# Optimization experiments

Measured on AMD Instinct MI355X. Metric: run time of the kernel, lower is better.

Reference implementation:

```python
import jax, jax.numpy as jnp
import numpy as np

B, T, S, H = 32, 1, 4096, 1024

def setup_inputs() -> dict:
    key = jax.random.key(0)
    ks = jax.random.split(key, 8)
    query = jax.random.normal(ks[0], (B, T, H), dtype=jnp.float32)
    encoder_outputs = jax.random.normal(ks[1], (B, S, H), dtype=jnp.float32)
    src_lengths = jax.random.randint(ks[2], (B,), 1, S + 1, dtype=jnp.int64)
    sc = 1.0 / np.sqrt(H)
    Ws_w = jax.random.normal(ks[3], (H, H), dtype=jnp.float32) * sc   # torch Linear weight (out,in)
    Wh_w = jax.random.normal(ks[4], (H, H), dtype=jnp.float32) * sc
    v_w = jax.random.normal(ks[5], (1, H), dtype=jnp.float32) * sc
    Wout_w = jax.random.normal(ks[6], (H, 2 * H), dtype=jnp.float32) * sc
    return {"query": query, "encoder_outputs": encoder_outputs, "src_lengths": src_lengths,
            "Ws_w": Ws_w, "Wh_w": Wh_w, "v_w": v_w, "Wout_w": Wout_w}

def reference(query, encoder_outputs, src_lengths, Ws_w, Wh_w, v_w, Wout_w):
    # score(h, s) = v^T tanh(Ws q + Wh h); query is a single decoder step (T=1)
    q_proj = jnp.einsum('bth,oh->bto', query, Ws_w)            # (B,1,H)
    h_proj = jnp.einsum('bsh,oh->bso', encoder_outputs, Wh_w)  # (B,S,H)
    scores = jnp.einsum('bsh,h->bs', jnp.tanh(q_proj + h_proj), v_w[0])  # (B,S)
    # NOTE: original calls non-in-place masked_fill and discards the result,
    # so src_lengths has no effect on the output (replicated faithfully).
    attn = jax.nn.softmax(scores, axis=-1)                     # (B,S)
    ctx = jnp.einsum('bs,bsh->bh', attn, encoder_outputs)[:, None, :]  # (B,1,H)
    cat = jnp.concatenate([ctx, query], axis=-1)               # (B,1,2H)
    return jnp.tanh(jnp.einsum('btk,ok->bto', cat, Wout_w))    # (B,1,H)
```

## Files before the change

kernel.cpp:

```cpp
#include <hip/hip_runtime.h>
#include <hip/hip_bf16.h>

#define B_  32
#define S_  4096
#define H_  1024
#define M_  (B_*S_)

typedef __attribute__((ext_vector_type(8))) short bf16x8;
typedef __attribute__((ext_vector_type(4))) float f32x4;

typedef void __attribute__((address_space(3)))* lds_ptr_t;
typedef void __attribute__((address_space(1)))* gbl_ptr_t;

__device__ __forceinline__ unsigned short f2bf(float x) {
    return __builtin_bit_cast(unsigned short, __float2bfloat16(x));
}

__device__ __forceinline__ float tanh_fast(float x) {
    float e = __expf(2.0f * x);
    return 1.0f - 2.0f / (e + 1.0f);
}

__global__ __launch_bounds__(256) void k_cvt_bf16(const float* __restrict__ in,
                                                  unsigned short* __restrict__ out, int n4) {
    int i = blockIdx.x * 256 + threadIdx.x;
    if (i < n4) {
        float4 f = reinterpret_cast<const float4*>(in)[i];
        ushort4 u;
        u.x = f2bf(f.x); u.y = f2bf(f.y); u.z = f2bf(f.z); u.w = f2bf(f.w);
        reinterpret_cast<ushort4*>(out)[i] = u;
    }
}

__global__ __launch_bounds__(256) void k_qproj(const float* __restrict__ q,
                                               const float* __restrict__ Ws,
                                               float* __restrict__ qp) {
    const int b = blockIdx.y, oc = blockIdx.x, tid = threadIdx.x;
    __shared__ float ql[H_];
    for (int i = tid; i < H_; i += 256) ql[i] = q[b*H_ + i];
    __syncthreads();
    const int o = oc*256 + tid;
    const float4* w = reinterpret_cast<const float4*>(&Ws[(size_t)o * H_]);
    float acc = 0.f;
    #pragma unroll 4
    for (int k4 = 0; k4 < H_/4; ++k4) {
        float4 ww = w[k4];
        acc += ql[k4*4+0]*ww.x + ql[k4*4+1]*ww.y + ql[k4*4+2]*ww.z + ql[k4*4+3]*ww.w;
    }
    qp[b*H_ + o] = acc;
}

__global__ __launch_bounds__(256) void k_scores(const float* __restrict__ enc,
                                                const unsigned short* __restrict__ whb,
                                                const float* __restrict__ qp,
                                                const float* __restrict__ vw,
                                                float* __restrict__ sp) {
    __shared__ __align__(16) unsigned short As[2][128][32];
    __shared__ __align__(16) unsigned short Bs[2][128][32];
    __shared__ float sred[2][128];

    const int tid  = threadIdx.x;
    const int lane = tid & 63;
    const int wid  = tid >> 6;
    const int wr = wid >> 1, wc = wid & 1;
    const int fr = lane & 15;
    const int fk = (lane >> 4) * 8;

    const int bn = blockIdx.x;
    const int bm = blockIdx.y;
    const int row0 = bm * 128;
    const int col0 = bn * 128;
    const int b = row0 >> 12;

    const int ar = tid >> 3;
    const int ak = (tid & 7) * 4;
    const int bnr = tid >> 2;
    const int bkk = (tid & 3) * 8;

    float4 areg[4];

    auto loadA = [&](int kt) {
        #pragma unroll
        for (int p = 0; p < 4; ++p)
            areg[p] = *reinterpret_cast<const float4*>(
                &enc[(size_t)(row0 + p*32 + ar) * H_ + kt*32 + ak]);
    };
    auto writeA = [&](int buf) {
        #pragma unroll
        for (int p = 0; p < 4; ++p) {
            ushort4 u;
            u.x = f2bf(areg[p].x); u.y = f2bf(areg[p].y);
            u.z = f2bf(areg[p].z); u.w = f2bf(areg[p].w);
            *reinterpret_cast<ushort4*>(&As[buf][p*32 + ar][ak]) = u;
        }
    };
    auto stageB = [&](int buf, int kt) {
        const unsigned short* g0 = whb + (size_t)(col0 + bnr) * H_ + kt*32 + bkk;
        const unsigned short* g1 = g0 + (size_t)64 * H_;
        char* l0 = (char*)(&Bs[buf][0][0]) + tid*16;
        __builtin_amdgcn_global_load_lds((gbl_ptr_t)g0, (lds_ptr_t)l0,        16, 0, 0);
        __builtin_amdgcn_global_load_lds((gbl_ptr_t)g1, (lds_ptr_t)(l0+4096), 16, 0, 0);
    };

    f32x4 acc[4][4] = {};

    loadA(0);
    stageB(0, 0);
    writeA(0);
    __syncthreads();

    for (int kt = 0; kt < 32; ++kt) {
        const int cur = kt & 1, nxt = cur ^ 1;
        if (kt < 31) { stageB(nxt, kt + 1); loadA(kt + 1); }

        bf16x8 af[4], bfr[4];
        #pragma unroll
        for (int i = 0; i < 4; ++i) {
            af[i]  = *reinterpret_cast<const bf16x8*>(&As[cur][wr*64 + i*16 + fr][fk]);
            bfr[i] = *reinterpret_cast<const bf16x8*>(&Bs[cur][wc*64 + i*16 + fr][fk]);
        }
        #pragma unroll
        for (int i = 0; i < 4; ++i)
            #pragma unroll
            for (int j = 0; j < 4; ++j)
                acc[i][j] = __builtin_amdgcn_mfma_f32_16x16x32_bf16(af[i], bfr[j], acc[i][j], 0, 0, 0);

        if (kt < 31) writeA(nxt);
        __syncthreads();
    }

    float vv[4], qq[4];
    #pragma unroll
    for (int j = 0; j < 4; ++j) {
        int c = col0 + wc*64 + j*16 + fr;
        vv[j] = vw[c];
        qq[j] = qp[b*H_ + c];
    }
    #pragma unroll
    for (int i = 0; i < 4; ++i) {
        #pragma unroll
        for (int r = 0; r < 4; ++r) {
            float s = 0.f;
            #pragma unroll
            for (int j = 0; j < 4; ++j)
                s += vv[j] * tanh_fast(qq[j] + acc[i][j][r]);
            #pragma unroll
            for (int m = 1; m < 16; m <<= 1)
                s += __shfl_xor(s, m, 64);
            if (fr == 0)
                sred[wc][wr*64 + i*16 + (lane >> 4)*4 + r] = s;
        }
    }
    __syncthreads();
    if (tid < 128)
        sp[(size_t)bn * M_ + row0 + tid] = sred[0][tid] + sred[1][tid];
}

__global__ __launch_bounds__(256) void k_softmax(const float* __restrict__ sp,
                                                 float* __restrict__ attn) {
    const int b = blockIdx.x, tid = threadIdx.x;
    __shared__ float red[4];
    float vals[16];
    float mx = -1e30f;
    #pragma unroll
    for (int i = 0; i < 16; ++i) {
        int s = i*256 + tid;
        float x = 0.f;
        #pragma unroll
        for (int p = 0; p < 8; ++p) x += sp[(size_t)p*M_ + b*S_ + s];
        vals[i] = x;
        mx = fmaxf(mx, x);
    }
    #pragma unroll
    for (int m = 1; m < 64; m <<= 1) mx = fmaxf(mx, __shfl_xor(mx, m, 64));
    if ((tid & 63) == 0) red[tid >> 6] = mx;
    __syncthreads();
    mx = fmaxf(fmaxf(red[0], red[1]), fmaxf(red[2], red[3]));
    float sum = 0.f;
    #pragma unroll
    for (int i = 0; i < 16; ++i) { vals[i] = __expf(vals[i] - mx); sum += vals[i]; }
    #pragma unroll
    for (int m = 1; m < 64; m <<= 1) sum += __shfl_xor(sum, m, 64);
    __syncthreads();
    if ((tid & 63) == 0) red[tid >> 6] = sum;
    __syncthreads();
    sum = red[0] + red[1] + red[2] + red[3];
    float inv = 1.f / sum;
    #pragma unroll
    for (int i = 0; i < 16; ++i) attn[b*S_ + i*256 + tid] = vals[i] * inv;
}

__global__ __launch_bounds__(256) void k_ctx(const float* __restrict__ attn,
                                             const float* __restrict__ enc,
                                             float* __restrict__ ctxp) {
    const int sc = blockIdx.x;
    const int b  = blockIdx.y;
    const int h  = threadIdx.x * 4;
    float ax = 0.f, ay = 0.f, az = 0.f, aw = 0.f;
    const int s0 = sc * 256;
    #pragma unroll 4
    for (int s = s0; s < s0 + 256; ++s) {
        float a = attn[b*S_ + s];
        float4 e = *reinterpret_cast<const float4*>(&enc[((size_t)b*S_ + s) * H_ + h]);
        ax += a*e.x; ay += a*e.y; az += a*e.z; aw += a*e.w;
    }
    float4 o; o.x = ax; o.y = ay; o.z = az; o.w = aw;
    *reinterpret_cast<float4*>(&ctxp[((size_t)sc*B_ + b) * H_ + h]) = o;
}

__global__ __launch_bounds__(256) void k_out(const float* __restrict__ ctxp,
                                             const float* __restrict__ q,
                                             const float* __restrict__ Wout,
                                             float* __restrict__ out) {
    const int oc = blockIdx.x, b = blockIdx.y, tid = threadIdx.x;
    __shared__ float cat[2*H_];
    for (int k = tid; k < H_; k += 256) {
        float s = 0.f;
        #pragma unroll
        for (int p = 0; p < 16; ++p) s += ctxp[((size_t)p*B_ + b) * H_ + k];
        cat[k] = s;
        cat[H_ + k] = q[b*H_ + k];
    }
    __syncthreads();
    const int o = oc*256 + tid;
    const float4* w = reinterpret_cast<const float4*>(&Wout[(size_t)o * 2*H_]);
    float acc = 0.f;
    #pragma unroll 4
    for (int k4 = 0; k4 < 2*H_/4; ++k4) {
        float4 ww = w[k4];
        acc += cat[k4*4+0]*ww.x + cat[k4*4+1]*ww.y + cat[k4*4+2]*ww.z + cat[k4*4+3]*ww.w;
    }
    out[b*H_ + o] = tanh_fast(acc);
}

extern "C" void kernel_launch(void* const* d_in, const int* in_sizes, int n_in,
                              void* d_out, int out_size, void* d_ws, size_t ws_size,
                              hipStream_t stream) {
    const float* query = (const float*)d_in[0];
    const float* enc   = (const float*)d_in[1];
    const float* Ws    = (const float*)d_in[3];
    const float* Wh    = (const float*)d_in[4];
    const float* vw    = (const float*)d_in[5];
    const float* Wout  = (const float*)d_in[6];
    float* out = (float*)d_out;

    char* ws = (char*)d_ws;
    unsigned short* whb = (unsigned short*)ws;
    float* sp   = (float*)(ws + (2u  << 20));
    float* attn = (float*)(ws + (6u  << 20));
    float* qp   = (float*)(ws + (6u  << 20) + (512u << 10));
    float* ctxp = (float*)(ws + (7u  << 20));

    k_cvt_bf16<<<dim3(1024),   dim3(256), 0, stream>>>(Wh, whb, H_*H_/4);
    k_qproj   <<<dim3(4, 32),  dim3(256), 0, stream>>>(query, Ws, qp);
    k_scores  <<<dim3(8, 1024),dim3(256), 0, stream>>>(enc, whb, qp, vw, sp);
    k_softmax <<<dim3(32),     dim3(256), 0, stream>>>(sp, attn);
    k_ctx     <<<dim3(16, 32), dim3(256), 0, stream>>>(attn, enc, ctxp);
    k_out     <<<dim3(4, 32),  dim3(256), 0, stream>>>(ctxp, query, Wout, out);
}
```

Baseline: 782.9 us.

## Pre-convert encoder outputs to bf16 and stage GEMM tiles via direct global-to-LDS loads

Adds a pass that converts the whole fp32 encoder tensor to bf16 in workspace. The scores GEMM then streams bf16 A tiles with global_load_lds, and the context reduction reads bf16 instead of fp32. This removes the per-tile fp32-to-bf16 conversion and eight-fold re-reads of fp32 data across the column blocks. It also remaps the 1D grid so blocks sharing rows run together for L2 reuse. The cost is an extra 512MB read plus 256MB write for conversion, a workspace requirement of about 266MB, and bf16 rounding in the context sum.

```diff
diff --git a/kernel.cpp b/kernel.cpp
--- a/kernel.cpp
+++ b/kernel.cpp
@@ -8,6 +8,7 @@
 
 typedef __attribute__((ext_vector_type(8))) short bf16x8;
 typedef __attribute__((ext_vector_type(4))) float f32x4;
+typedef __attribute__((ext_vector_type(8))) unsigned short ushort8;
 
 typedef void __attribute__((address_space(3)))* lds_ptr_t;
 typedef void __attribute__((address_space(1)))* gbl_ptr_t;
@@ -15,7 +16,9 @@
 __device__ __forceinline__ unsigned short f2bf(float x) {
     return __builtin_bit_cast(unsigned short, __float2bfloat16(x));
 }
-
+__device__ __forceinline__ float bf2f(unsigned short u) {
+    return __builtin_bit_cast(float, (unsigned)u << 16);
+}
 __device__ __forceinline__ float tanh_fast(float x) {
     float e = __expf(2.0f * x);
     return 1.0f - 2.0f / (e + 1.0f);
@@ -32,6 +35,19 @@
     }
 }
 
+__global__ __launch_bounds__(256) void k_cvt_enc(const float* __restrict__ in,
+                                                 unsigned short* __restrict__ out, int n8) {
+    const int stride = gridDim.x * 256;
+    for (int i = blockIdx.x * 256 + threadIdx.x; i < n8; i += stride) {
+        float4 a = reinterpret_cast<const float4*>(in)[(size_t)i * 2];
+        float4 b = reinterpret_cast<const float4*>(in)[(size_t)i * 2 + 1];
+        ushort8 u;
+        u[0] = f2bf(a.x); u[1] = f2bf(a.y); u[2] = f2bf(a.z); u[3] = f2bf(a.w);
+        u[4] = f2bf(b.x); u[5] = f2bf(b.y); u[6] = f2bf(b.z); u[7] = f2bf(b.w);
+        reinterpret_cast<ushort8*>(out)[i] = u;
+    }
+}
+
 __global__ __launch_bounds__(256) void k_qproj(const float* __restrict__ q,
                                                const float* __restrict__ Ws,
                                                float* __restrict__ qp) {
@@ -50,11 +66,11 @@
     qp[b*H_ + o] = acc;
 }
 
-__global__ __launch_bounds__(256) void k_scores(const float* __restrict__ enc,
-                                                const unsigned short* __restrict__ whb,
-                                                const float* __restrict__ qp,
-                                                const float* __restrict__ vw,
-                                                float* __restrict__ sp) {
+__global__ __launch_bounds__(256) void k_scores_b(const unsigned short* __restrict__ encb,
+                                                  const unsigned short* __restrict__ whb,
+                                                  const float* __restrict__ qp,
+                                                  const float* __restrict__ vw,
+                                                  float* __restrict__ sp) {
     __shared__ __align__(16) unsigned short As[2][128][32];
     __shared__ __align__(16) unsigned short Bs[2][128][32];
     __shared__ float sred[2][128];
@@ -66,8 +82,99 @@
     const int fr = lane & 15;
     const int fk = (lane >> 4) * 8;
 
-    const int bn = blockIdx.x;
-    const int bm = blockIdx.y;
+    const int h  = blockIdx.x;
+    const int L  = (h & 7) * 1024 + (h >> 3);
+    const int bm = L >> 3;
+    const int bn = L & 7;
+    const int row0 = bm * 128;
+    const int col0 = bn * 128;
+    const int b = row0 >> 12;
+
+    const int sr = tid >> 2;
+    const int sk = (tid & 3) * 8;
+
+    auto stage = [&](int buf, int kt) {
+        const unsigned short* ga0 = encb + (size_t)(row0 + sr) * H_ + kt*32 + sk;
+        const unsigned short* gb0 = whb  + (size_t)(col0 + sr) * H_ + kt*32 + sk;
+        char* la = (char*)(&As[buf][0][0]) + tid*16;
+        char* lb = (char*)(&Bs[buf][0][0]) + tid*16;
+        __builtin_amdgcn_global_load_lds((gbl_ptr_t)ga0,                 (lds_ptr_t)la,        16, 0, 0);
+        __builtin_amdgcn_global_load_lds((gbl_ptr_t)(ga0 + (size_t)64*H_),(lds_ptr_t)(la+4096), 16, 0, 0);
+        __builtin_amdgcn_global_load_lds((gbl_ptr_t)gb0,                 (lds_ptr_t)lb,        16, 0, 0);
+        __builtin_amdgcn_global_load_lds((gbl_ptr_t)(gb0 + (size_t)64*H_),(lds_ptr_t)(lb+4096), 16, 0, 0);
+    };
+
+    f32x4 acc[4][4] = {};
+
+    stage(0, 0);
+    __syncthreads();
+
+    for (int kt = 0; kt < 32; ++kt) {
+        const int cur = kt & 1, nxt = cur ^ 1;
+        if (kt < 31) stage(nxt, kt + 1);
+
+        bf16x8 af[4], bfr[4];
+        #pragma unroll
+        for (int i = 0; i < 4; ++i) {
+            af[i]  = *reinterpret_cast<const bf16x8*>(&As[cur][wr*64 + i*16 + fr][fk]);
+            bfr[i] = *reinterpret_cast<const bf16x8*>(&Bs[cur][wc*64 + i*16 + fr][fk]);
+        }
+        #pragma unroll
+        for (int i = 0; i < 4; ++i)
+            #pragma unroll
+            for (int j = 0; j < 4; ++j)
+                acc[i][j] = __builtin_amdgcn_mfma_f32_16x16x32_bf16(af[i], bfr[j], acc[i][j], 0, 0, 0);
+
+        __syncthreads();
+    }
+
+    float vv[4], qq[4];
+    #pragma unroll
+    for (int j = 0; j < 4; ++j) {
+        int c = col0 + wc*64 + j*16 + fr;
+        vv[j] = vw[c];
+        qq[j] = qp[b*H_ + c];
+    }
+    #pragma unroll
+    for (int i = 0; i < 4; ++i) {
+        #pragma unroll
+        for (int r = 0; r < 4; ++r) {
+            float s = 0.f;
+            #pragma unroll
+            for (int j = 0; j < 4; ++j)
+                s += vv[j] * tanh_fast(qq[j] + acc[i][j][r]);
+            #pragma unroll
+            for (int m = 1; m < 16; m <<= 1)
+                s += __shfl_xor(s, m, 64);
+            if (fr == 0)
+                sred[wc][wr*64 + i*16 + (lane >> 4)*4 + r] = s;
+        }
+    }
+    __syncthreads();
+    if (tid < 128)
+        sp[(size_t)bn * M_ + row0 + tid] = sred[0][tid] + sred[1][tid];
+}
+
+__global__ __launch_bounds__(256) void k_scores_f(const float* __restrict__ enc,
+                                                  const unsigned short* __restrict__ whb,
+                                                  const float* __restrict__ qp,
+                                                  const float* __restrict__ vw,
+                                                  float* __restrict__ sp) {
+    __shared__ __align__(16) unsigned short As[2][128][32];
+    __shared__ __align__(16) unsigned short Bs[2][128][32];
+    __shared__ float sred[2][128];
+
+    const int tid  = threadIdx.x;
+    const int lane = tid & 63;
+    const int wid  = tid >> 6;
+    const int wr = wid >> 1, wc = wid & 1;
+    const int fr = lane & 15;
+    const int fk = (lane >> 4) * 8;
+
+    const int h  = blockIdx.x;
+    const int L  = (h & 7) * 1024 + (h >> 3);
+    const int bm = L >> 3;
+    const int bn = L & 7;
     const int row0 = bm * 128;
     const int col0 = bn * 128;
     const int b = row0 >> 12;
@@ -78,7 +185,6 @@
     const int bkk = (tid & 3) * 8;
 
     float4 areg[4];
-
     auto loadA = [&](int kt) {
         #pragma unroll
         for (int p = 0; p < 4; ++p)
@@ -190,22 +296,40 @@
     for (int i = 0; i < 16; ++i) attn[b*S_ + i*256 + tid] = vals[i] * inv;
 }
 
-__global__ __launch_bounds__(256) void k_ctx(const float* __restrict__ attn,
-                                             const float* __restrict__ enc,
-                                             float* __restrict__ ctxp) {
+__global__ __launch_bounds__(256) void k_ctx_b(const float* __restrict__ attn,
+                                               const unsigned short* __restrict__ encb,
+                                               float* __restrict__ ctxp) {
     const int sc = blockIdx.x;
     const int b  = blockIdx.y;
-    const int h  = threadIdx.x * 4;
+    const int hh = threadIdx.x * 4;
     float ax = 0.f, ay = 0.f, az = 0.f, aw = 0.f;
     const int s0 = sc * 256;
     #pragma unroll 4
     for (int s = s0; s < s0 + 256; ++s) {
         float a = attn[b*S_ + s];
-        float4 e = *reinterpret_cast<const float4*>(&enc[((size_t)b*S_ + s) * H_ + h]);
+        ushort4 e = *reinterpret_cast<const ushort4*>(&encb[((size_t)b*S_ + s) * H_ + hh]);
+        ax += a*bf2f(e.x); ay += a*bf2f(e.y); az += a*bf2f(e.z); aw += a*bf2f(e.w);
+    }
+    float4 o; o.x = ax; o.y = ay; o.z = az; o.w = aw;
+    *reinterpret_cast<float4*>(&ctxp[((size_t)sc*B_ + b) * H_ + hh]) = o;
+}
+
+__global__ __launch_bounds__(256) void k_ctx_f(const float* __restrict__ attn,
+                                               const float* __restrict__ enc,
+                                               float* __restrict__ ctxp) {
+    const int sc = blockIdx.x;
+    const int b  = blockIdx.y;
+    const int hh = threadIdx.x * 4;
+    float ax = 0.f, ay = 0.f, az = 0.f, aw = 0.f;
+    const int s0 = sc * 256;
+    #pragma unroll 4
+    for (int s = s0; s < s0 + 256; ++s) {
+        float a = attn[b*S_ + s];
+        float4 e = *reinterpret_cast<const float4*>(&enc[((size_t)b*S_ + s) * H_ + hh]);
         ax += a*e.x; ay += a*e.y; az += a*e.z; aw += a*e.w;
     }
     float4 o; o.x = ax; o.y = ay; o.z = az; o.w = aw;
-    *reinterpret_cast<float4*>(&ctxp[((size_t)sc*B_ + b) * H_ + h]) = o;
+    *reinterpret_cast<float4*>(&ctxp[((size_t)sc*B_ + b) * H_ + hh]) = o;
 }
 
 __global__ __launch_bounds__(256) void k_out(const float* __restrict__ ctxp,
@@ -245,16 +369,34 @@
     float* out = (float*)d_out;
 
     char* ws = (char*)d_ws;
-    unsigned short* whb = (unsigned short*)ws;
-    float* sp   = (float*)(ws + (2u  << 20));
-    float* attn = (float*)(ws + (6u  << 20));
-    float* qp   = (float*)(ws + (6u  << 20) + (512u << 10));
-    float* ctxp = (float*)(ws + (7u  << 20));
-
-    k_cvt_bf16<<<dim3(1024),   dim3(256), 0, stream>>>(Wh, whb, H_*H_/4);
-    k_qproj   <<<dim3(4, 32),  dim3(256), 0, stream>>>(query, Ws, qp);
-    k_scores  <<<dim3(8, 1024),dim3(256), 0, stream>>>(enc, whb, qp, vw, sp);
-    k_softmax <<<dim3(32),     dim3(256), 0, stream>>>(sp, attn);
-    k_ctx     <<<dim3(16, 32), dim3(256), 0, stream>>>(attn, enc, ctxp);
-    k_out     <<<dim3(4, 32),  dim3(256), 0, stream>>>(ctxp, query, Wout, out);
-}
+
+    if (ws_size >= (266ull << 20)) {
+        unsigned short* encb = (unsigned short*)ws;
+        unsigned short* whb  = (unsigned short*)(ws + (256ull << 20));
+        float* sp   = (float*)(ws + (258ull << 20));
+        float* attn = (float*)(ws + (262ull << 20));
+        float* qp   = (float*)(ws + (262ull << 20) + (512u << 10));
+        float* ctxp = (float*)(ws + (263ull << 20));
+
+        k_cvt_enc <<<dim3(2048),    dim3(256), 0, stream>>>(enc, encb, M_*H_/8);
+        k_cvt_bf16<<<dim3(1024),    dim3(256), 0, stream>>>(Wh, whb, H_*H_/4);
+        k_qproj   <<<dim3(4, 32),   dim3(256), 0, stream>>>(query, Ws, qp);
+        k_scores_b<<<dim3(8192),    dim3(256), 0, stream>>>(encb, whb, qp, vw, sp);
+        k_softmax <<<dim3(32),      dim3(256), 0, stream>>>(sp, attn);
+        k_ctx_b   <<<dim3(16, 32),  dim3(256), 0, stream>>>(attn, encb, ctxp);
+        k_out     <<<dim3(4, 32),   dim3(256), 0, stream>>>(ctxp, query, Wout, out);
+    } else {
+        unsigned short* whb = (unsigned short*)ws;
+        float* sp   = (float*)(ws + (2u  << 20));
+        float* attn = (float*)(ws + (6u  << 20));
+        float* qp   = (float*)(ws + (6u  << 20) + (512u << 10));
+        float* ctxp = (float*)(ws + (7u  << 20));
+
+        k_cvt_bf16<<<dim3(1024),    dim3(256), 0, stream>>>(Wh, whb, H_*H_/4);
+        k_qproj   <<<dim3(4, 32),   dim3(256), 0, stream>>>(query, Ws, qp);
+        k_scores_f<<<dim3(8192),    dim3(256), 0, stream>>>(enc, whb, qp, vw, sp);
+        k_softmax <<<dim3(32),      dim3(256), 0, stream>>>(sp, attn);
+        k_ctx_f   <<<dim3(16, 32),  dim3(256), 0, stream>>>(attn, enc, ctxp);
+        k_out     <<<dim3(4, 32),   dim3(256), 0, stream>>>(ctxp, query, Wout, out);
+    }
+}
```

Measured after the change: 672.0 us. 14.2% less time.

## Rewrite scores GEMM with fragment-native LDS layout and deeper prefetch pipeline

Applied to the files above, without the earlier changes.

Rewrites the scores GEMM kernel. LDS tiles are now laid out in MFMA fragment order, A is prefetched two stages ahead in registers, and B uses a triple-buffered global_load_lds ring. Syncs are manual waitcnt plus s_barrier, MFMA blocks are wrapped in s_setprio, and the 1-D grid is remapped so blocks sharing the same column tile of Wh are spread across the launch order. The aim is to hide global-load latency, avoid LDS bank conflicts, and raise occupancy via launch bounds (256,3), at the cost of more registers and fragile hand-tuned wait counts.

```diff
diff --git a/kernel.cpp b/kernel.cpp
--- a/kernel.cpp
+++ b/kernel.cpp
@@ -8,6 +8,7 @@
 
 typedef __attribute__((ext_vector_type(8))) short bf16x8;
 typedef __attribute__((ext_vector_type(4))) float f32x4;
+typedef __attribute__((ext_vector_type(8))) unsigned short ushort8;
 
 typedef void __attribute__((address_space(3)))* lds_ptr_t;
 typedef void __attribute__((address_space(1)))* gbl_ptr_t;
@@ -15,7 +16,6 @@
 __device__ __forceinline__ unsigned short f2bf(float x) {
     return __builtin_bit_cast(unsigned short, __float2bfloat16(x));
 }
-
 __device__ __forceinline__ float tanh_fast(float x) {
     float e = __expf(2.0f * x);
     return 1.0f - 2.0f / (e + 1.0f);
@@ -50,114 +50,144 @@
     qp[b*H_ + o] = acc;
 }
 
-__global__ __launch_bounds__(256) void k_scores(const float* __restrict__ enc,
-                                                const unsigned short* __restrict__ whb,
-                                                const float* __restrict__ qp,
-                                                const float* __restrict__ vw,
-                                                float* __restrict__ sp) {
-    __shared__ __align__(16) unsigned short As[2][128][32];
-    __shared__ __align__(16) unsigned short Bs[2][128][32];
-    __shared__ float sred[2][128];
-
-    const int tid  = threadIdx.x;
-    const int lane = tid & 63;
-    const int wid  = tid >> 6;
-    const int wr = wid >> 1, wc = wid & 1;
-    const int fr = lane & 15;
-    const int fk = (lane >> 4) * 8;
-
-    const int bn = blockIdx.x;
-    const int bm = blockIdx.y;
+__global__ __launch_bounds__(256, 3) void k_scores_r(const float* __restrict__ enc,
+                                                     const unsigned short* __restrict__ whb,
+                                                     const float* __restrict__ qp,
+                                                     const float* __restrict__ vw,
+                                                     float* __restrict__ sp) {
+    __shared__ __align__(1024) char smem[40960];
+
+    const int tid = threadIdx.x;
+    const int l   = tid & 63;
+    const int w   = tid >> 6;
+    const int wr  = w >> 1;
+    const int wc  = w & 1;
+    const int fr  = l & 15;
+    const int fh  = l >> 4;
+
+    const int hb = blockIdx.x;
+    const int L  = (hb & 7) * 1024 + (hb >> 3);
+    const int bm = L >> 3;
+    const int bn = L & 7;
     const int row0 = bm * 128;
     const int col0 = bn * 128;
     const int b = row0 >> 12;
 
-    const int ar = tid >> 3;
-    const int ak = (tid & 7) * 4;
-    const int bnr = tid >> 2;
-    const int bkk = (tid & 3) * 8;
-
-    float4 areg[4];
-
-    auto loadA = [&](int kt) {
-        #pragma unroll
-        for (int p = 0; p < 4; ++p)
-            areg[p] = *reinterpret_cast<const float4*>(
-                &enc[(size_t)(row0 + p*32 + ar) * H_ + kt*32 + ak]);
-    };
-    auto writeA = [&](int buf) {
-        #pragma unroll
-        for (int p = 0; p < 4; ++p) {
-            ushort4 u;
-            u.x = f2bf(areg[p].x); u.y = f2bf(areg[p].y);
-            u.z = f2bf(areg[p].z); u.w = f2bf(areg[p].w);
-            *reinterpret_cast<ushort4*>(&As[buf][p*32 + ar][ak]) = u;
-        }
-    };
-    auto stageB = [&](int buf, int kt) {
-        const unsigned short* g0 = whb + (size_t)(col0 + bnr) * H_ + kt*32 + bkk;
-        const unsigned short* g1 = g0 + (size_t)64 * H_;
-        char* l0 = (char*)(&Bs[buf][0][0]) + tid*16;
-        __builtin_amdgcn_global_load_lds((gbl_ptr_t)g0, (lds_ptr_t)l0,        16, 0, 0);
-        __builtin_amdgcn_global_load_lds((gbl_ptr_t)g1, (lds_ptr_t)(l0+4096), 16, 0, 0);
-    };
-
-    f32x4 acc[4][4] = {};
-
-    loadA(0);
-    stageB(0, 0);
-    writeA(0);
-    __syncthreads();
-
-    for (int kt = 0; kt < 32; ++kt) {
-        const int cur = kt & 1, nxt = cur ^ 1;
-        if (kt < 31) { stageB(nxt, kt + 1); loadA(kt + 1); }
-
-        bf16x8 af[4], bfr[4];
-        #pragma unroll
-        for (int i = 0; i < 4; ++i) {
-            af[i]  = *reinterpret_cast<const bf16x8*>(&As[cur][wr*64 + i*16 + fr][fk]);
-            bfr[i] = *reinterpret_cast<const bf16x8*>(&Bs[cur][wc*64 + i*16 + fr][fk]);
-        }
-        #pragma unroll
-        for (int i = 0; i < 4; ++i)
+    const float* srcA[2];
+    #pragma unroll
+    for (int sub = 0; sub < 2; ++sub) {
+        const int rblk = sub*4 + w;
+        srcA[sub] = enc + (size_t)(row0 + rblk*16 + fr) * H_ + fh*8;
+    }
+    const unsigned short* srcB[2];
+    #pragma unroll
+    for (int j = 0; j < 2; ++j) {
+        const int nblk = j*4 + w;
+        srcB[j] = whb + (size_t)(col0 + nblk*16 + fr) * H_ + fh*8;
+    }
+
+    float4 fset[2][2][2];
+
+    auto loadA = [&](int t, int set) {
+        #pragma unroll
+        for (int sub = 0; sub < 2; ++sub) {
+            fset[set][sub][0] = *reinterpret_cast<const float4*>(srcA[sub] + t*32);
+            fset[set][sub][1] = *reinterpret_cast<const float4*>(srcA[sub] + t*32 + 4);
+        }
+    };
+    auto stageB = [&](int t) {
+        #pragma unroll
+        for (int j = 0; j < 2; ++j)
+            __builtin_amdgcn_global_load_lds((gbl_ptr_t)(srcB[j] + t*32),
+                (lds_ptr_t)(smem + 16384 + (t % 3)*8192 + (j*4 + w)*1024 + l*16), 16, 0, 0);
+    };
+    auto cvtWrite = [&](int set, int buf) {
+        #pragma unroll
+        for (int sub = 0; sub < 2; ++sub) {
+            ushort8 u;
             #pragma unroll
-            for (int j = 0; j < 4; ++j)
-                acc[i][j] = __builtin_amdgcn_mfma_f32_16x16x32_bf16(af[i], bfr[j], acc[i][j], 0, 0, 0);
-
-        if (kt < 31) writeA(nxt);
-        __syncthreads();
-    }
+            for (int hlf = 0; hlf < 2; ++hlf) {
+                float4 f = fset[set][sub][hlf];
+                u[hlf*4+0] = f2bf(f.x); u[hlf*4+1] = f2bf(f.y);
+                u[hlf*4+2] = f2bf(f.z); u[hlf*4+3] = f2bf(f.w);
+            }
+            *reinterpret_cast<ushort8*>(smem + buf*8192 + (sub*4 + w)*1024 + l*16) = u;
+        }
+    };
+
+    f32x4  acc[4][4] = {};
+    bf16x8 af[4], ba[4];
+
+    auto ldFrags = [&](int t) {
+        #pragma unroll
+        for (int m2 = 0; m2 < 4; ++m2)
+            af[m2] = *reinterpret_cast<const bf16x8*>(
+                smem + (t & 1)*8192 + (wr*4 + m2)*1024 + l*16);
+        #pragma unroll
+        for (int n2 = 0; n2 < 4; ++n2)
+            ba[n2] = *reinterpret_cast<const bf16x8*>(
+                smem + 16384 + (t % 3)*8192 + (wc*4 + n2)*1024 + l*16);
+    };
+    auto mfma16 = [&] {
+        __builtin_amdgcn_s_setprio(1);
+        #pragma unroll
+        for (int m2 = 0; m2 < 4; ++m2)
+            #pragma unroll
+            for (int n2 = 0; n2 < 4; ++n2)
+                acc[m2][n2] = __builtin_amdgcn_mfma_f32_16x16x32_bf16(
+                    af[m2], ba[n2], acc[m2][n2], 0, 0, 0);
+        __builtin_amdgcn_s_setprio(0);
+    };
+    auto barrier = [] { asm volatile("s_barrier" ::: "memory"); };
+
+    loadA(0, 0); stageB(0); loadA(1, 1); stageB(1);
+    asm volatile("s_waitcnt vmcnt(2)" ::: "memory");
+    cvtWrite(0, 0);
+    asm volatile("s_waitcnt lgkmcnt(0)" ::: "memory");
+    barrier();
+
+    #pragma unroll
+    for (int t = 0; t < 32; ++t) {
+        ldFrags(t);
+        if (t <= 29) { loadA(t+2, t & 1); stageB(t+2); }
+        mfma16();
+        if (t <= 29)      asm volatile("s_waitcnt vmcnt(6)" ::: "memory");
+        else if (t == 30) asm volatile("s_waitcnt vmcnt(0)" ::: "memory");
+        if (t <= 30) {
+            cvtWrite((t+1) & 1, (t+1) & 1);
+            asm volatile("s_waitcnt lgkmcnt(0)" ::: "memory");
+        }
+        if (t <= 30) barrier();
+    }
+    __syncthreads();
 
     float vv[4], qq[4];
     #pragma unroll
-    for (int j = 0; j < 4; ++j) {
-        int c = col0 + wc*64 + j*16 + fr;
-        vv[j] = vw[c];
-        qq[j] = qp[b*H_ + c];
-    }
-    #pragma unroll
-    for (int i = 0; i < 4; ++i) {
+    for (int n = 0; n < 4; ++n) {
+        int c = col0 + wc*64 + n*16 + fr;
+        vv[n] = vw[c];
+        qq[n] = qp[b*H_ + c];
+    }
+    float* sred = (float*)smem;
+    #pragma unroll
+    for (int m2 = 0; m2 < 4; ++m2)
         #pragma unroll
         for (int r = 0; r < 4; ++r) {
             float s = 0.f;
             #pragma unroll
-            for (int j = 0; j < 4; ++j)
-                s += vv[j] * tanh_fast(qq[j] + acc[i][j][r]);
-            #pragma unroll
-            for (int m = 1; m < 16; m <<= 1)
-                s += __shfl_xor(s, m, 64);
-            if (fr == 0)
-                sred[wc][wr*64 + i*16 + (lane >> 4)*4 + r] = s;
-        }
-    }
+            for (int n = 0; n < 4; ++n)
+                s += vv[n] * tanh_fast(qq[n] + acc[m2][n][r]);
+            s += __shfl_xor(s, 1, 64); s += __shfl_xor(s, 2, 64);
+            s += __shfl_xor(s, 4, 64); s += __shfl_xor(s, 8, 64);
+            if (fr == 0) sred[wc*128 + wr*64 + m2*16 + fh*4 + r] = s;
+        }
     __syncthreads();
     if (tid < 128)
-        sp[(size_t)bn * M_ + row0 + tid] = sred[0][tid] + sred[1][tid];
+        sp[(size_t)bn * M_ + row0 + tid] = sred[tid] + sred[128 + tid];
 }
 
 __global__ __launch_bounds__(256) void k_softmax(const float* __restrict__ sp,
-                                                 float* __restrict__ attn) {
+                                                 float* __restrict__ attn, int P) {
     const int b = blockIdx.x, tid = threadIdx.x;
     __shared__ float red[4];
     float vals[16];
@@ -166,8 +196,7 @@
     for (int i = 0; i < 16; ++i) {
         int s = i*256 + tid;
         float x = 0.f;
-        #pragma unroll
-        for (int p = 0; p < 8; ++p) x += sp[(size_t)p*M_ + b*S_ + s];
+        for (int p = 0; p < P; ++p) x += sp[(size_t)p*M_ + b*S_ + s];
         vals[i] = x;
         mx = fmaxf(mx, x);
     }
@@ -190,22 +219,22 @@
     for (int i = 0; i < 16; ++i) attn[b*S_ + i*256 + tid] = vals[i] * inv;
 }
 
-__global__ __launch_bounds__(256) void k_ctx(const float* __restrict__ attn,
-                                             const float* __restrict__ enc,
-                                             float* __restrict__ ctxp) {
+__global__ __launch_bounds__(256) void k_ctx_f(const float* __restrict__ attn,
+                                               const float* __restrict__ enc,
+                                               float* __restrict__ ctxp) {
     const int sc = blockIdx.x;
     const int b  = blockIdx.y;
-    const int h  = threadIdx.x * 4;
+    const int hh = threadIdx.x * 4;
     float ax = 0.f, ay = 0.f, az = 0.f, aw = 0.f;
     const int s0 = sc * 256;
     #pragma unroll 4
     for (int s = s0; s < s0 + 256; ++s) {
         float a = attn[b*S_ + s];
-        float4 e = *reinterpret_cast<const float4*>(&enc[((size_t)b*S_ + s) * H_ + h]);
+        float4 e = *reinterpret_cast<const float4*>(&enc[((size_t)b*S_ + s) * H_ + hh]);
         ax += a*e.x; ay += a*e.y; az += a*e.z; aw += a*e.w;
     }
     float4 o; o.x = ax; o.y = ay; o.z = az; o.w = aw;
-    *reinterpret_cast<float4*>(&ctxp[((size_t)sc*B_ + b) * H_ + h]) = o;
+    *reinterpret_cast<float4*>(&ctxp[((size_t)sc*B_ + b) * H_ + hh]) = o;
 }
 
 __global__ __launch_bounds__(256) void k_out(const float* __restrict__ ctxp,
@@ -253,8 +282,8 @@
 
     k_cvt_bf16<<<dim3(1024),   dim3(256), 0, stream>>>(Wh, whb, H_*H_/4);
     k_qproj   <<<dim3(4, 32),  dim3(256), 0, stream>>>(query, Ws, qp);
-    k_scores  <<<dim3(8, 1024),dim3(256), 0, stream>>>(enc, whb, qp, vw, sp);
-    k_softmax <<<dim3(32),     dim3(256), 0, stream>>>(sp, attn);
-    k_ctx     <<<dim3(16, 32), dim3(256), 0, stream>>>(attn, enc, ctxp);
+    k_scores_r<<<dim3(8192),   dim3(256), 0, stream>>>(enc, whb, qp, vw, sp);
+    k_softmax <<<dim3(32),     dim3(256), 0, stream>>>(sp, attn, 8);
+    k_ctx_f   <<<dim3(16, 32), dim3(256), 0, stream>>>(attn, enc, ctxp);
     k_out     <<<dim3(4, 32),  dim3(256), 0, stream>>>(ctxp, query, Wout, out);
 }
```

After: 974.3 us. +24.5%, slower.

## Stage fp32 encoder tiles directly to LDS with swizzle and remap block order

Applied to the files above, without the earlier changes.

The scores GEMM now loads the fp32 encoder A-tile straight into LDS with global_load_lds instead of going through registers, and converts to bf16 when reading MFMA fragments. LDS addresses are XOR-style rotated per row to avoid bank conflicts, and the grid is flattened with a remapping so the 8 column blocks that share an A row-tile are spread across the launch order. The aim is to remove the register round trip and the conversion store on the load path, and to improve L2 behaviour. In exchange, LDS for A doubles and each fragment read now performs the conversion on every k-step.

```diff
diff --git a/kernel.cpp b/kernel.cpp
--- a/kernel.cpp
+++ b/kernel.cpp
@@ -15,7 +15,6 @@
 __device__ __forceinline__ unsigned short f2bf(float x) {
     return __builtin_bit_cast(unsigned short, __float2bfloat16(x));
 }
-
 __device__ __forceinline__ float tanh_fast(float x) {
     float e = __expf(2.0f * x);
     return 1.0f - 2.0f / (e + 1.0f);
@@ -50,82 +49,95 @@
     qp[b*H_ + o] = acc;
 }
 
-__global__ __launch_bounds__(256) void k_scores(const float* __restrict__ enc,
-                                                const unsigned short* __restrict__ whb,
-                                                const float* __restrict__ qp,
-                                                const float* __restrict__ vw,
-                                                float* __restrict__ sp) {
-    __shared__ __align__(16) unsigned short As[2][128][32];
-    __shared__ __align__(16) unsigned short Bs[2][128][32];
+__global__ __launch_bounds__(256) void k_scores_v(const float* __restrict__ enc,
+                                                  const unsigned short* __restrict__ whb,
+                                                  const float* __restrict__ qp,
+                                                  const float* __restrict__ vw,
+                                                  float* __restrict__ sp) {
+    __shared__ __align__(1024) char As[2][16384];
+    __shared__ __align__(1024) char Bs[2][8192];
     __shared__ float sred[2][128];
 
-    const int tid  = threadIdx.x;
-    const int lane = tid & 63;
-    const int wid  = tid >> 6;
-    const int wr = wid >> 1, wc = wid & 1;
-    const int fr = lane & 15;
-    const int fk = (lane >> 4) * 8;
-
-    const int bn = blockIdx.x;
-    const int bm = blockIdx.y;
+    const int tid = threadIdx.x;
+    const int l   = tid & 63;
+    const int w   = tid >> 6;
+    const int wr  = w >> 1;
+    const int wc  = w & 1;
+    const int fr  = l & 15;
+    const int fh  = l >> 4;
+
+    const int h  = blockIdx.x;
+    const int L  = (h & 7) * 1024 + (h >> 3);
+    const int bm = L >> 3;
+    const int bn = L & 7;
     const int row0 = bm * 128;
     const int col0 = bn * 128;
     const int b = row0 >> 12;
 
-    const int ar = tid >> 3;
-    const int ak = (tid & 7) * 4;
-    const int bnr = tid >> 2;
-    const int bkk = (tid & 3) * 8;
-
-    float4 areg[4];
-
-    auto loadA = [&](int kt) {
-        #pragma unroll
-        for (int p = 0; p < 4; ++p)
-            areg[p] = *reinterpret_cast<const float4*>(
-                &enc[(size_t)(row0 + p*32 + ar) * H_ + kt*32 + ak]);
+    const int arow   = tid >> 3;
+    const int achunk = ((tid & 7) - (tid >> 3)) & 7;
+    const float* srcA[4];
+    #pragma unroll
+    for (int i = 0; i < 4; ++i)
+        srcA[i] = enc + (size_t)(row0 + i*32 + arow) * H_ + achunk*4;
+
+    const int brow   = tid >> 2;
+    const int bchunk = ((tid & 3) - ((tid >> 3) & 3)) & 3;
+    const unsigned short* srcB[2];
+    #pragma unroll
+    for (int j = 0; j < 2; ++j)
+        srcB[j] = whb + (size_t)(col0 + j*64 + brow) * H_ + bchunk*8;
+
+    auto stage = [&](int buf, int kt) {
+        #pragma unroll
+        for (int i = 0; i < 4; ++i)
+            __builtin_amdgcn_global_load_lds((gbl_ptr_t)(srcA[i] + kt*32),
+                (lds_ptr_t)(&As[buf][i*4096 + tid*16]), 16, 0, 0);
+        #pragma unroll
+        for (int j = 0; j < 2; ++j)
+            __builtin_amdgcn_global_load_lds((gbl_ptr_t)(srcB[j] + kt*32),
+                (lds_ptr_t)(&Bs[buf][j*4096 + tid*16]), 16, 0, 0);
     };
-    auto writeA = [&](int buf) {
-        #pragma unroll
-        for (int p = 0; p < 4; ++p) {
-            ushort4 u;
-            u.x = f2bf(areg[p].x); u.y = f2bf(areg[p].y);
-            u.z = f2bf(areg[p].z); u.w = f2bf(areg[p].w);
-            *reinterpret_cast<ushort4*>(&As[buf][p*32 + ar][ak]) = u;
-        }
+
+    const int aOff0 = wr*8192 + fr*128 + (((fh*2 + 0) + (l & 7)) & 7)*16;
+    const int aOff1 = wr*8192 + fr*128 + (((fh*2 + 1) + (l & 7)) & 7)*16;
+    const int bOff  = wc*4096 + fr*64 + ((fh + (fr >> 1)) & 3)*16;
+
+    auto cvt8 = [](f32x4 x, f32x4 y) -> bf16x8 {
+        bf16x8 r;
+        r[0] = (short)f2bf(x[0]); r[1] = (short)f2bf(x[1]);
+        r[2] = (short)f2bf(x[2]); r[3] = (short)f2bf(x[3]);
+        r[4] = (short)f2bf(y[0]); r[5] = (short)f2bf(y[1]);
+        r[6] = (short)f2bf(y[2]); r[7] = (short)f2bf(y[3]);
+        return r;
     };
-    auto stageB = [&](int buf, int kt) {
-        const unsigned short* g0 = whb + (size_t)(col0 + bnr) * H_ + kt*32 + bkk;
-        const unsigned short* g1 = g0 + (size_t)64 * H_;
-        char* l0 = (char*)(&Bs[buf][0][0]) + tid*16;
-        __builtin_amdgcn_global_load_lds((gbl_ptr_t)g0, (lds_ptr_t)l0,        16, 0, 0);
-        __builtin_amdgcn_global_load_lds((gbl_ptr_t)g1, (lds_ptr_t)(l0+4096), 16, 0, 0);
-    };
 
     f32x4 acc[4][4] = {};
 
-    loadA(0);
-    stageB(0, 0);
-    writeA(0);
+    stage(0, 0);
     __syncthreads();
 
     for (int kt = 0; kt < 32; ++kt) {
         const int cur = kt & 1, nxt = cur ^ 1;
-        if (kt < 31) { stageB(nxt, kt + 1); loadA(kt + 1); }
-
-        bf16x8 af[4], bfr[4];
-        #pragma unroll
-        for (int i = 0; i < 4; ++i) {
-            af[i]  = *reinterpret_cast<const bf16x8*>(&As[cur][wr*64 + i*16 + fr][fk]);
-            bfr[i] = *reinterpret_cast<const bf16x8*>(&Bs[cur][wc*64 + i*16 + fr][fk]);
+        if (kt < 31) stage(nxt, kt + 1);
+
+        bf16x8 af[4], ba[4];
+        #pragma unroll
+        for (int m2 = 0; m2 < 4; ++m2) {
+            f32x4 x = *reinterpret_cast<const f32x4*>(&As[cur][aOff0 + m2*2048]);
+            f32x4 y = *reinterpret_cast<const f32x4*>(&As[cur][aOff1 + m2*2048]);
+            af[m2] = cvt8(x, y);
         }
+        #pragma unroll
+        for (int n2 = 0; n2 < 4; ++n2)
+            ba[n2] = *reinterpret_cast<const bf16x8*>(&Bs[cur][bOff + n2*1024]);
+
         #pragma unroll
         for (int i = 0; i < 4; ++i)
             #pragma unroll
             for (int j = 0; j < 4; ++j)
-                acc[i][j] = __builtin_amdgcn_mfma_f32_16x16x32_bf16(af[i], bfr[j], acc[i][j], 0, 0, 0);
-
-        if (kt < 31) writeA(nxt);
+                acc[i][j] = __builtin_amdgcn_mfma_f32_16x16x32_bf16(af[i], ba[j], acc[i][j], 0, 0, 0);
+
         __syncthreads();
     }
 
@@ -144,11 +156,10 @@
             #pragma unroll
             for (int j = 0; j < 4; ++j)
                 s += vv[j] * tanh_fast(qq[j] + acc[i][j][r]);
-            #pragma unroll
-            for (int m = 1; m < 16; m <<= 1)
-                s += __shfl_xor(s, m, 64);
+            s += __shfl_xor(s, 1, 64); s += __shfl_xor(s, 2, 64);
+            s += __shfl_xor(s, 4, 64); s += __shfl_xor(s, 8, 64);
             if (fr == 0)
-                sred[wc][wr*64 + i*16 + (lane >> 4)*4 + r] = s;
+                sred[wc][wr*64 + i*16 + fh*4 + r] = s;
         }
     }
     __syncthreads();
@@ -190,22 +201,22 @@
     for (int i = 0; i < 16; ++i) attn[b*S_ + i*256 + tid] = vals[i] * inv;
 }
 
-__global__ __launch_bounds__(256) void k_ctx(const float* __restrict__ attn,
-                                             const float* __restrict__ enc,
-                                             float* __restrict__ ctxp) {
+__global__ __launch_bounds__(256) void k_ctx_f(const float* __restrict__ attn,
+                                               const float* __restrict__ enc,
+                                               float* __restrict__ ctxp) {
     const int sc = blockIdx.x;
     const int b  = blockIdx.y;
-    const int h  = threadIdx.x * 4;
+    const int hh = threadIdx.x * 4;
     float ax = 0.f, ay = 0.f, az = 0.f, aw = 0.f;
     const int s0 = sc * 256;
     #pragma unroll 4
     for (int s = s0; s < s0 + 256; ++s) {
         float a = attn[b*S_ + s];
-        float4 e = *reinterpret_cast<const float4*>(&enc[((size_t)b*S_ + s) * H_ + h]);
+        float4 e = *reinterpret_cast<const float4*>(&enc[((size_t)b*S_ + s) * H_ + hh]);
         ax += a*e.x; ay += a*e.y; az += a*e.z; aw += a*e.w;
     }
     float4 o; o.x = ax; o.y = ay; o.z = az; o.w = aw;
-    *reinterpret_cast<float4*>(&ctxp[((size_t)sc*B_ + b) * H_ + h]) = o;
+    *reinterpret_cast<float4*>(&ctxp[((size_t)sc*B_ + b) * H_ + hh]) = o;
 }
 
 __global__ __launch_bounds__(256) void k_out(const float* __restrict__ ctxp,
@@ -253,8 +264,8 @@
 
     k_cvt_bf16<<<dim3(1024),   dim3(256), 0, stream>>>(Wh, whb, H_*H_/4);
     k_qproj   <<<dim3(4, 32),  dim3(256), 0, stream>>>(query, Ws, qp);
-    k_scores  <<<dim3(8, 1024),dim3(256), 0, stream>>>(enc, whb, qp, vw, sp);
+    k_scores_v<<<dim3(8192),   dim3(256), 0, stream>>>(enc, whb, qp, vw, sp);
     k_softmax <<<dim3(32),     dim3(256), 0, stream>>>(sp, attn);
-    k_ctx     <<<dim3(16, 32), dim3(256), 0, stream>>>(attn, enc, ctxp);
+    k_ctx_f   <<<dim3(16, 32), dim3(256), 0, stream>>>(attn, enc, ctxp);
     k_out     <<<dim3(4, 32),  dim3(256), 0, stream>>>(ctxp, query, Wout, out);
 }
```

After: 859.4 us. +9.8%, slower.
